# Optimization experiments

Hardware: AMD Instinct MI355X
Metric: run time of the kernel (lower is better)

Reference implementation:

```python
import jax, jax.numpy as jnp
import numpy as np

N_NODES = 100000
N_EDGES = 1600000
N_GRAPHS = 1024
EMB = 32
HID = 64
N_CLASSES = 10
N_SHAPE = 16
N_COLOR = 8


def setup_inputs() -> dict:
    key = jax.random.key(0)
    ks = jax.random.split(key, 12)
    shape_id = jax.random.randint(ks[0], (N_NODES,), 0, N_SHAPE + 1, dtype=jnp.int32)
    color_id = jax.random.randint(ks[1], (N_NODES,), 0, N_COLOR + 1, dtype=jnp.int32)
    edge_index = jax.random.randint(ks[2], (2, N_EDGES), 0, N_NODES, dtype=jnp.int32)
    batch = jnp.sort(jax.random.randint(ks[3], (N_NODES,), 0, N_GRAPHS, dtype=jnp.int32))
    shape_table = jax.random.normal(ks[4], (N_SHAPE + 1, EMB), jnp.float32)
    color_table = jax.random.normal(ks[5], (N_COLOR + 1, EMB), jnp.float32)
    W1 = jax.random.normal(ks[6], (EMB, HID), jnp.float32) / np.sqrt(EMB)
    b1 = jnp.zeros((HID,), jnp.float32)
    W2 = jax.random.normal(ks[7], (HID, HID), jnp.float32) / np.sqrt(HID)
    b2 = jnp.zeros((HID,), jnp.float32)
    Wl = jax.random.normal(ks[8], (HID, N_CLASSES), jnp.float32) / np.sqrt(HID)
    bl = jnp.zeros((N_CLASSES,), jnp.float32)
    return dict(shape_id=shape_id, color_id=color_id, edge_index=edge_index, batch=batch,
                shape_table=shape_table, color_table=color_table,
                W1=W1, b1=b1, W2=W2, b2=b2, Wl=Wl, bl=bl)


def gcn_conv(x, W, b, src, dst, num_nodes):
    # PyG GCNConv: add self-loops, symmetric normalization D^-1/2 (A+I) D^-1/2
    h = x @ W  # [N, out]
    deg = 1.0 + jax.ops.segment_sum(jnp.ones_like(dst, jnp.float32), dst, num_segments=num_nodes)
    dis = jax.lax.rsqrt(deg)  # deg >= 1 due to self-loop
    norm = dis[src] * dis[dst]  # [E]
    agg = jax.ops.segment_sum(h[src] * norm[:, None], dst, num_segments=num_nodes)
    agg = agg + h * (dis * dis)[:, None]  # self-loop term
    return agg + b


def reference(shape_id, color_id, edge_index, batch, shape_table, color_table,
              W1, b1, W2, b2, Wl, bl):
    # padding_idx=0 -> row 0 contributes zeros
    st = shape_table.at[0].set(0.0)
    ct = color_table.at[0].set(0.0)
    x = st[shape_id] + ct[color_id]  # [N, emb]
    src, dst = edge_index[0], edge_index[1]
    x = jax.nn.relu(gcn_conv(x, W1, b1, src, dst, N_NODES))
    x = jax.nn.relu(gcn_conv(x, W2, b2, src, dst, N_NODES))
    # global_mean_pool over batch ids
    sums = jax.ops.segment_sum(x, batch, num_segments=N_GRAPHS)
    cnts = jax.ops.segment_sum(jnp.ones((x.shape[0],), x.dtype), batch, num_segments=N_GRAPHS)
    pooled = sums / jnp.maximum(cnts, 1.0)[:, None]  # [B, hidden]
    return pooled @ Wl + bl  # [B, num_classes]
```

## Files before the change

### kernel.cpp

```cpp
#include <hip/hip_runtime.h>
#include <hip/hip_bf16.h>
#include <hip/hip_fp16.h>

#define N_NODES   100000
#define N_EDGES   1600000
#define N_GRAPHS  1024
#define EMB       32
#define HID       64
#define N_CLASSES 10
#define SCAN_BLOCKS 391
#define NCOMBO 153
#define BUCK_NODES 448
#define NBUCK 224
#define BIN_CAP 8192
#define EPB 4096
#define PBCAP 11328
#define SENTINEL N_NODES
#define NTILES 6250
#define AGG_GRID 3125

typedef _Float16 f16x8 __attribute__((ext_vector_type(8)));
typedef float f32x4 __attribute__((ext_vector_type(4)));

__global__ __launch_bounds__(256) void prep_kernel(
    const int* __restrict__ sid, const int* __restrict__ cid,
    const int* __restrict__ batch, int* __restrict__ combo, int* __restrict__ gstart,
    const float* __restrict__ st, const float* __restrict__ ct,
    const float* __restrict__ W1, __half* __restrict__ TCh,
    float* __restrict__ pooled, int* __restrict__ gcur, __half* __restrict__ h2s) {
    int t = threadIdx.x;
    int v = blockIdx.x * 256 + t;
    if (v < N_GRAPHS * HID) pooled[v] = 0.0f;
    if (blockIdx.x == 0) {
        if (t < NBUCK) gcur[t] = 0;
        if (t == 0) combo[N_NODES] = 0;
        if (t < 32) ((float*)(h2s + (size_t)N_NODES * HID))[t] = 0.0f;
    }
    if (v < N_NODES) {
        combo[v] = sid[v] * 9 + cid[v];
        int b = batch[v];
        int bp = (v == 0) ? -1 : batch[v - 1];
        for (int g = bp + 1; g <= b; ++g) gstart[g] = v;
        if (v == N_NODES - 1) {
            for (int g = b + 1; g <= N_GRAPHS; ++g) gstart[g] = N_NODES;
        }
    }
    if (blockIdx.x < NCOMBO && t >= 64 && t < 128) {
        int r = blockIdx.x, j = t - 64;
        int s = r / 9, c = r % 9;
        float acc = 0.0f;
        if (s != 0) {
#pragma unroll
            for (int k = 0; k < EMB; ++k) acc = fmaf(st[s * EMB + k], W1[k * HID + j], acc);
        }
        if (c != 0) {
#pragma unroll
            for (int k = 0; k < EMB; ++k) acc = fmaf(ct[c * EMB + k], W1[k * HID + j], acc);
        }
        TCh[r * HID + j] = __float2half_rn(acc);
    }
}

__global__ __launch_bounds__(512) void binA_kernel(
    const int* __restrict__ src, const int* __restrict__ dst,
    int* __restrict__ gcur, int* __restrict__ gbin) {
    __shared__ int2 stg[EPB];
    __shared__ int hist[NBUCK];
    __shared__ int base[NBUCK + 1];
    __shared__ int gstart[NBUCK];
    __shared__ int scanbuf[256];
    int t = threadIdx.x;
    int e0 = blockIdx.x * EPB;
    for (int i = t; i < NBUCK; i += 512) hist[i] = 0;
    __syncthreads();

    int2 myq[8];
    int mybo[8];
    if (e0 + EPB <= N_EDGES) {
        int eb = e0 + t * 8;
        int4 sa4 = *(const int4*)&src[eb];
        int4 sb4 = *(const int4*)&src[eb + 4];
        int4 da4 = *(const int4*)&dst[eb];
        int4 db4 = *(const int4*)&dst[eb + 4];
        int ss[8] = {sa4.x, sa4.y, sa4.z, sa4.w, sb4.x, sb4.y, sb4.z, sb4.w};
        int dd[8] = {da4.x, da4.y, da4.z, da4.w, db4.x, db4.y, db4.z, db4.w};
#pragma unroll
        for (int i = 0; i < 8; ++i) {
            unsigned b = (unsigned)dd[i] / BUCK_NODES;
            int off = atomicAdd(&hist[b], 1);
            myq[i].x = ss[i];
            myq[i].y = dd[i];
            mybo[i] = (int)(b << 16) | off;
        }
    } else {
#pragma unroll
        for (int i = 0; i < 8; ++i) {
            int e = e0 + t * 8 + i;
            if (e < N_EDGES) {
                int d = dst[e];
                unsigned b = (unsigned)d / BUCK_NODES;
                int off = atomicAdd(&hist[b], 1);
                myq[i].x = src[e];
                myq[i].y = d;
                mybo[i] = (int)(b << 16) | off;
            } else {
                mybo[i] = -1;
            }
        }
    }
    __syncthreads();

    int h = (t < NBUCK) ? hist[t] : 0;
    if (t < 256) scanbuf[t] = h;
    __syncthreads();
#pragma unroll
    for (int off = 1; off < 256; off <<= 1) {
        int x = (t < 256 && t >= off) ? scanbuf[t - off] : 0;
        __syncthreads();
        if (t < 256) scanbuf[t] += x;
        __syncthreads();
    }
    if (t < NBUCK) base[t] = scanbuf[t] - h;
    if (t == 0) base[NBUCK] = scanbuf[255];
    __syncthreads();
#pragma unroll
    for (int i = 0; i < 8; ++i) {
        if (mybo[i] >= 0) {
            int b = mybo[i] >> 16, off = mybo[i] & 0xFFFF;
            stg[base[b] + off] = myq[i];
        }
    }
    if (t < NBUCK) {
        int n = hist[t];
        gstart[t] = n ? atomicAdd(&gcur[t], n) : 0;
    }
    __syncthreads();
    int total = base[NBUCK];
    for (int i = t; i < total; i += 512) {
        int2 q = stg[i];
        unsigned b = (unsigned)q.y / BUCK_NODES;
        int local = q.y - (int)b * BUCK_NODES;
        gbin[(size_t)b * BIN_CAP + gstart[b] + (i - base[b])] = q.x | (local << 17);
    }
}

__global__ __launch_bounds__(1024) void bucket_scatter_kernel(
    const int* __restrict__ gbin, const int* __restrict__ gcur,
    float* __restrict__ dis, int* __restrict__ rowptr, int* __restrict__ epack4) {
    __shared__ __align__(16) int pbin[BIN_CAP];
    __shared__ int ldeg[BUCK_NODES];
    __shared__ int rbase[BUCK_NODES];
    __shared__ int s[512];
    int b = blockIdx.x, t = threadIdx.x;
    for (int i = t; i < BUCK_NODES; i += 1024) ldeg[i] = 0;
    __syncthreads();
    int n = gcur[b];
    int nc = (n + 3) >> 2;
    {
        const int4* my4 = (const int4*)(gbin + (size_t)b * BIN_CAP);
        for (int c = t; c < nc; c += 1024) {
            int4 p4 = my4[c];
            ((int4*)pbin)[c] = p4;
            int i0 = c * 4;
            if (i0 + 0 < n) atomicAdd(&ldeg[(unsigned)p4.x >> 17], 1);
            if (i0 + 1 < n) atomicAdd(&ldeg[(unsigned)p4.y >> 17], 1);
            if (i0 + 2 < n) atomicAdd(&ldeg[(unsigned)p4.z >> 17], 1);
            if (i0 + 3 < n) atomicAdd(&ldeg[(unsigned)p4.w >> 17], 1);
        }
    }
    __syncthreads();
    int d = (t < BUCK_NODES) ? ldeg[t] : 0;
    int v = b * BUCK_NODES + t;
    if (t < BUCK_NODES && v < N_NODES) dis[v] = rsqrtf(1.0f + (float)d);
    if (b == 0 && t == 0) dis[N_NODES] = 0.0f;
    int dp = (d + 7) & ~7;
    if (dp > 248) dp = 248;
    if (t < 512) s[t] = dp;
    __syncthreads();
#pragma unroll
    for (int off = 1; off < 512; off <<= 1) {
        int x = (t < 512 && t >= off) ? s[t - off] : 0;
        __syncthreads();
        if (t < 512) s[t] += x;
        __syncthreads();
    }
    int rp = 0;
    if (t < 512) rp = b * PBCAP + s[t] - dp;
    if (t < BUCK_NODES) {
        rbase[t] = rp;
        if (v < N_NODES) rowptr[v] = rp | (dp << 24);
    }
    for (int i = t; i < BUCK_NODES; i += 1024) ldeg[i] = 0;
    __syncthreads();
    if (t < BUCK_NODES) {
        for (int k = d; k < dp; ++k) epack4[rp + k] = SENTINEL;
    }
    for (int i = t; i < n; i += 1024) {
        int p = pbin[i];
        int local = (unsigned)p >> 17;
        int r = atomicAdd(&ldeg[local], 1);
        if (r < 248) epack4[rbase[local] + r] = p & 0x1FFFF;
    }
}

#define AGG_CHUNK(CQ, DQ, LBASE)                                               \
    _Pragma("unroll")                                                          \
    for (int i = 0; i < 8; ++i) {                                              \
        int off = __builtin_amdgcn_readlane((CQ), (LBASE) + i);                \
        int wb  = __builtin_amdgcn_readlane(__float_as_int(DQ), (LBASE) + i);  \
        __half tv = *(const __half*)((const char*)TCs + (off + lane2));        \
        acc = fmaf(__int_as_float(wb), __half2float(tv), acc);                 \
    }

#define AGG_NODE(N, RP, DEG, DV, CO)                                           \
    {                                                                          \
        int deg = (DEG);                                                       \
        int cnt = deg > 32 ? 32 : deg;                                         \
        float acc = 0.0f;                                                      \
        if (cnt > 0)  { AGG_CHUNK(cq1, dq1, (N)*16) }                          \
        if (cnt > 8)  { AGG_CHUNK(cq1, dq1, (N)*16 + 8) }                      \
        if (cnt > 16) { AGG_CHUNK(cq2, dq2, (N)*16) }                          \
        if (cnt > 24) { AGG_CHUNK(cq2, dq2, (N)*16 + 8) }                      \
        if (deg > 32) {                                                        \
            for (int e = (RP) + 32; e < (RP) + deg; ++e) {                     \
                int qx = epack4[e] & 0x1FFFF;                                  \
                float dw = dis[qx];                                            \
                __half tv = *(const __half*)((const char*)TCs +                \
                                             ((combo[qx] << 7) + lane2));      \
                acc = fmaf(dw, __half2float(tv), acc);                         \
            }                                                                  \
        }                                                                      \
        __half hv = *(const __half*)((const char*)TCs + ((CO) + lane2));       \
        float val = (DV) * fmaf(__half2float(hv), (DV), acc) + bias;           \
        val = val > 0.0f ? val : 0.0f;                                         \
        xsA[w * 4 + (N)][lane] = __float2half_rn(val * (DV));                  \
    }

__global__ __launch_bounds__(256, 7) void agg1_mm2_kernel(
    const int* __restrict__ epack4, const int* __restrict__ rowptr,
    const int* __restrict__ combo, const float* __restrict__ dis,
    const __half* __restrict__ TCh, const float* __restrict__ W2,
    const float* __restrict__ b1, __half* __restrict__ h2s) {
    __shared__ __align__(16) __half TCs[NCOMBO * HID];
    __shared__ __align__(16) __half xsA[16][72];
    int t = threadIdx.x;
    int lane = t & 63, w = t >> 6;
    int lane2 = lane * 2;
    int sub = lane >> 4, sl = lane & 15;

    int tile = blockIdx.x;
    int v0 = tile * 16 + w * 4;
    {
    }
    int rb = rowptr[v0 + sub] & 0xFFFFFF;
    int q1x = epack4[rb + sl] & 0x1FFFF;
    int q2x = epack4[rb + 16 + sl] & 0x1FFFF;
    float dq1 = dis[q1x], dq2 = dis[q2x];
    int cq1 = combo[q1x] << 7, cq2 = combo[q2x] << 7;
    int r0p = __builtin_amdgcn_readfirstlane(rowptr[v0]);
    int r1p = __builtin_amdgcn_readfirstlane(rowptr[v0 + 1]);
    int r2p = __builtin_amdgcn_readfirstlane(rowptr[v0 + 2]);
    int r3p = __builtin_amdgcn_readfirstlane(rowptr[v0 + 3]);
    float d0 = dis[v0], d1 = dis[v0 + 1], d2 = dis[v0 + 2], d3 = dis[v0 + 3];
    int o0 = combo[v0] << 7, o1 = combo[v0 + 1] << 7;
    int o2 = combo[v0 + 2] << 7, o3 = combo[v0 + 3] << 7;

    float bias = b1[lane];
    f16x8 bf0, bf1;
    {
        int colw = (w << 4) + (lane & 15);
        int kb = (lane >> 4) * 8;
#pragma unroll
        for (int i = 0; i < 8; ++i) {
            bf0[i] = (_Float16)W2[(kb + i) * HID + colw];
            bf1[i] = (_Float16)W2[(32 + kb + i) * HID + colw];
        }
    }
    {
        const int4* s4 = (const int4*)TCh;
        int4* dd4 = (int4*)TCs;
        for (int i = t; i < NCOMBO * HID * 2 / 16; i += 256) dd4[i] = s4[i];
    }
    __syncthreads();

    for (;;) {
        int ntile = tile + AGG_GRID;
        bool more = ntile < NTILES;
        int nv0 = 0, nq1x = 0, nq2x = 0;
        int nr0p = 0, nr1p = 0, nr2p = 0, nr3p = 0;
        float ndq1 = 0.0f, ndq2 = 0.0f, nd0 = 0.0f, nd1 = 0.0f, nd2 = 0.0f, nd3 = 0.0f;
        int ncq1 = 0, ncq2 = 0, no0 = 0, no1 = 0, no2 = 0, no3 = 0;
        if (more) {
            nv0 = ntile * 16 + w * 4;
            int nrb = rowptr[nv0 + sub] & 0xFFFFFF;
            nq1x = epack4[nrb + sl] & 0x1FFFF;
            nq2x = epack4[nrb + 16 + sl] & 0x1FFFF;
            ndq1 = dis[nq1x]; ndq2 = dis[nq2x];
            ncq1 = combo[nq1x] << 7; ncq2 = combo[nq2x] << 7;
            nr0p = __builtin_amdgcn_readfirstlane(rowptr[nv0]);
            nr1p = __builtin_amdgcn_readfirstlane(rowptr[nv0 + 1]);
            nr2p = __builtin_amdgcn_readfirstlane(rowptr[nv0 + 2]);
            nr3p = __builtin_amdgcn_readfirstlane(rowptr[nv0 + 3]);
            nd0 = dis[nv0]; nd1 = dis[nv0 + 1]; nd2 = dis[nv0 + 2]; nd3 = dis[nv0 + 3];
            no0 = combo[nv0] << 7; no1 = combo[nv0 + 1] << 7;
            no2 = combo[nv0 + 2] << 7; no3 = combo[nv0 + 3] << 7;
        }
        int r0 = r0p & 0xFFFFFF, g0 = (int)((unsigned)r0p >> 24);
        int r1 = r1p & 0xFFFFFF, g1 = (int)((unsigned)r1p >> 24);
        int r2 = r2p & 0xFFFFFF, g2 = (int)((unsigned)r2p >> 24);
        int r3 = r3p & 0xFFFFFF, g3 = (int)((unsigned)r3p >> 24);
        AGG_NODE(0, r0, g0, d0, o0)
        AGG_NODE(1, r1, g1, d1, o1)
        AGG_NODE(2, r2, g2, d2, o2)
        AGG_NODE(3, r3, g3, d3, o3)
        __syncthreads();

        const __half* xa = &xsA[lane & 15][0];
        f16x8 a0 = *(const f16x8*)(xa + (lane >> 4) * 8);
        f16x8 a1 = *(const f16x8*)(xa + 32 + (lane >> 4) * 8);
        __syncthreads();
        f32x4 dacc = {0.0f, 0.0f, 0.0f, 0.0f};
        dacc = __builtin_amdgcn_mfma_f32_16x16x32_f16(a0, bf0, dacc, 0, 0, 0);
        dacc = __builtin_amdgcn_mfma_f32_16x16x32_f16(a1, bf1, dacc, 0, 0, 0);

        __half* Dst = (__half*)xsA;
        {
            int colg = (w << 4) + (lane & 15);
#pragma unroll
            for (int i = 0; i < 4; ++i)
                Dst[((lane >> 4) * 4 + i) * 64 + colg] = __float2half_rn(dacc[i]);
        }
        __syncthreads();

        {
            const uint2* ds2 = (const uint2*)Dst;
            uint2* go = (uint2*)(h2s + (size_t)tile * 16 * HID);
            go[t] = ds2[t];
        }
        if (!more) break;
        __syncthreads();
        tile = ntile; v0 = nv0;
        q1x = nq1x; q2x = nq2x; dq1 = ndq1; dq2 = ndq2; cq1 = ncq1; cq2 = ncq2;
        r0p = nr0p; r1p = nr1p; r2p = nr2p; r3p = nr3p;
        d0 = nd0; d1 = nd1; d2 = nd2; d3 = nd3;
        o0 = no0; o1 = no1; o2 = no2; o3 = no3;
    }
}

__device__ __forceinline__ float agg2_node(const int* __restrict__ epack4, int sx,
                                           int rs, int deg, int lane, int lane2,
                                           const __half* __restrict__ h2s) {
    float acc = 0.0f;
    int p = rs;
    int re = rs + deg;
    for (;;) {
        int avail = re - p;
        int cnt = avail > 64 ? 64 : avail;
        int vo = sx << 7;
        int j = 0;
        for (; j + 16 <= cnt; j += 16) {
            float g[16];
#pragma unroll
            for (int i = 0; i < 16; ++i) {
                int off = __builtin_amdgcn_readlane(vo, j + i);
                g[i] = __half2float(*(const __half*)((const char*)h2s + (off + lane2)));
            }
#pragma unroll
            for (int i = 0; i < 16; ++i) acc += g[i];
        }
        if (j < cnt) {
            float g[8];
#pragma unroll
            for (int i = 0; i < 8; ++i) {
                int off = __builtin_amdgcn_readlane(vo, j + i);
                g[i] = __half2float(*(const __half*)((const char*)h2s + (off + lane2)));
            }
#pragma unroll
            for (int i = 0; i < 8; ++i) acc += g[i];
        }
        p += 64;
        if (p >= re) break;
        sx = epack4[p + lane];
    }
    return acc;
}

__global__ __launch_bounds__(256, 8) void agg2_pool_kernel(
    const int* __restrict__ epack4, const int* __restrict__ rowptr,
    const __half* __restrict__ h2s, const float* __restrict__ dis,
    const float* __restrict__ b2, const int* __restrict__ batch,
    float* __restrict__ pooled) {
    int t = threadIdx.x, lane = t & 63, w = t >> 6;
    int lane2 = lane * 2;
    int v0 = (blockIdx.x * 4 + w) * 4;

    int r0p = __builtin_amdgcn_readfirstlane(rowptr[v0]);
    int r1p = __builtin_amdgcn_readfirstlane(rowptr[v0 + 1]);
    int r2p = __builtin_amdgcn_readfirstlane(rowptr[v0 + 2]);
    int r3p = __builtin_amdgcn_readfirstlane(rowptr[v0 + 3]);
    int r0 = r0p & 0xFFFFFF, dp0 = (int)((unsigned)r0p >> 24);
    int r1 = r1p & 0xFFFFFF, dp1 = (int)((unsigned)r1p >> 24);
    int r2 = r2p & 0xFFFFFF, dp2 = (int)((unsigned)r2p >> 24);
    int r3 = r3p & 0xFFFFFF, dp3 = (int)((unsigned)r3p >> 24);

    int sa = epack4[r0 + lane];
    int sb = epack4[r1 + lane];
    int sc = epack4[r2 + lane];
    int sd = epack4[r3 + lane];

    float bv = b2[lane];
    float acc0 = agg2_node(epack4, sa, r0, dp0, lane, lane2, h2s);
    float acc1 = agg2_node(epack4, sb, r1, dp1, lane, lane2, h2s);
    float acc2 = agg2_node(epack4, sc, r2, dp2, lane, lane2, h2s);
    float acc3 = agg2_node(epack4, sd, r3, dp3, lane, lane2, h2s);

#define AGG2_VAL(V, ACC, OUT)                                                  \
    {                                                                          \
        float dv = dis[V];                                                     \
        float self = __half2float(h2s[(size_t)(V) * HID + lane]);              \
        float val = dv * ((ACC) + self) + bv;                                  \
        OUT = val > 0.0f ? val : 0.0f;                                         \
    }
    float val0, val1, val2, val3;
    AGG2_VAL(v0, acc0, val0)
    AGG2_VAL(v0 + 1, acc1, val1)
    AGG2_VAL(v0 + 2, acc2, val2)
    AGG2_VAL(v0 + 3, acc3, val3)
#undef AGG2_VAL

    int g0 = __builtin_amdgcn_readfirstlane(batch[v0]);
    int g1 = __builtin_amdgcn_readfirstlane(batch[v0 + 1]);
    int g2 = __builtin_amdgcn_readfirstlane(batch[v0 + 2]);
    int g3 = __builtin_amdgcn_readfirstlane(batch[v0 + 3]);
    float s = val0; int g = g0;
    if (g1 == g) { s += val1; } else { unsafeAtomicAdd(&pooled[g * HID + lane], s); g = g1; s = val1; }
    if (g2 == g) { s += val2; } else { unsafeAtomicAdd(&pooled[g * HID + lane], s); g = g2; s = val2; }
    if (g3 == g) { s += val3; } else { unsafeAtomicAdd(&pooled[g * HID + lane], s); g = g3; s = val3; }
    unsafeAtomicAdd(&pooled[g * HID + lane], s);
}

__global__ __launch_bounds__(64) void logits_kernel(
    const float* __restrict__ pooled, const int* __restrict__ gstart,
    const float* __restrict__ Wl, const float* __restrict__ bl,
    float* __restrict__ out) {
    __shared__ float row[HID];
    int g = blockIdx.x, t = threadIdx.x;
    int c = gstart[g + 1] - gstart[g]; if (c < 1) c = 1;
    row[t] = pooled[g * HID + t] / (float)c;
    __syncthreads();
    if (t < N_CLASSES) {
        float acc = bl[t];
#pragma unroll
        for (int k = 0; k < HID; ++k) acc = fmaf(row[k], Wl[k * N_CLASSES + t], acc);
        out[g * N_CLASSES + t] = acc;
    }
}

extern "C" void kernel_launch(void* const* d_in, const int* in_sizes, int n_in,
                              void* d_out, int out_size, void* d_ws, size_t ws_size,
                              hipStream_t stream) {
    const int*   shape_id = (const int*)d_in[0];
    const int*   color_id = (const int*)d_in[1];
    const int*   edge_idx = (const int*)d_in[2];
    const int*   batch    = (const int*)d_in[3];
    const float* st       = (const float*)d_in[4];
    const float* ct       = (const float*)d_in[5];
    const float* W1       = (const float*)d_in[6];
    const float* b1       = (const float*)d_in[7];
    const float* W2       = (const float*)d_in[8];
    const float* b2       = (const float*)d_in[9];
    const float* Wl       = (const float*)d_in[10];
    const float* bl       = (const float*)d_in[11];
    float* out = (float*)d_out;

    const int* src = edge_idx;
    const int* dst = edge_idx + N_EDGES;

    char* ws = (char*)d_ws;
    int*    combo   = (int*)   (ws + 0);
    float*  dis     = (float*) (ws + 400384);
    int*    gstart  = (int*)   (ws + 801792);
    int*    rowptr  = (int*)   (ws + 1201152);
    __half* TCh     = (__half*)(ws + 1603584);
    float*  pooled  = (float*) (ws + 1623552);
    int*    gcur    = (int*)   (ws + 1889792);
    int*    epack4  = (int*)   (ws + 1890816);
    int*    gbin    = (int*)   (ws + 14690816);
    __half* h2s     = (__half*)(ws + 29370880);

    prep_kernel<<<SCAN_BLOCKS, 256, 0, stream>>>(shape_id, color_id, batch, combo, gstart,
                                                 st, ct, W1, TCh, pooled, gcur, h2s);

    binA_kernel<<<(N_EDGES + EPB - 1) / EPB, 512, 0, stream>>>(src, dst, gcur, gbin);

    bucket_scatter_kernel<<<NBUCK, 1024, 0, stream>>>(gbin, gcur, dis, rowptr, epack4);

    agg1_mm2_kernel<<<AGG_GRID, 256, 0, stream>>>(epack4, rowptr, combo, dis, TCh, W2, b1, h2s);

    agg2_pool_kernel<<<6250, 256, 0, stream>>>(epack4, rowptr, h2s, dis, b2, batch, pooled);

    logits_kernel<<<N_GRAPHS, 64, 0, stream>>>(pooled, gstart, Wl, bl, out);
}
```

Baseline: 176.1 us.

## Aggregate four nodes' edges as one contiguous stream in both GCN aggregation kernels

Both aggregation kernels now treat the padded edge rows of a warp's four nodes as one contiguous range. They process it in 64-edge windows, routing each 8-edge chunk sum to the owning node's accumulator via prefix offsets, and prefetch the next window's indices. This replaces per-node loops, the fixed 32-entry preload, and a separate overflow path. Fewer epack loads and less per-node branching are expected, at the cost of assuming the four rows are adjacent in memory and adding per-chunk selection logic.

```diff
diff --git a/kernel.cpp b/kernel.cpp
--- a/kernel.cpp
+++ b/kernel.cpp
@@ -203,39 +203,6 @@
     }
 }
 
-#define AGG_CHUNK(CQ, DQ, LBASE)                                               \
-    _Pragma("unroll")                                                          \
-    for (int i = 0; i < 8; ++i) {                                              \
-        int off = __builtin_amdgcn_readlane((CQ), (LBASE) + i);                \
-        int wb  = __builtin_amdgcn_readlane(__float_as_int(DQ), (LBASE) + i);  \
-        __half tv = *(const __half*)((const char*)TCs + (off + lane2));        \
-        acc = fmaf(__int_as_float(wb), __half2float(tv), acc);                 \
-    }
-
-#define AGG_NODE(N, RP, DEG, DV, CO)                                           \
-    {                                                                          \
-        int deg = (DEG);                                                       \
-        int cnt = deg > 32 ? 32 : deg;                                         \
-        float acc = 0.0f;                                                      \
-        if (cnt > 0)  { AGG_CHUNK(cq1, dq1, (N)*16) }                          \
-        if (cnt > 8)  { AGG_CHUNK(cq1, dq1, (N)*16 + 8) }                      \
-        if (cnt > 16) { AGG_CHUNK(cq2, dq2, (N)*16) }                          \
-        if (cnt > 24) { AGG_CHUNK(cq2, dq2, (N)*16 + 8) }                      \
-        if (deg > 32) {                                                        \
-            for (int e = (RP) + 32; e < (RP) + deg; ++e) {                     \
-                int qx = epack4[e] & 0x1FFFF;                                  \
-                float dw = dis[qx];                                            \
-                __half tv = *(const __half*)((const char*)TCs +                \
-                                             ((combo[qx] << 7) + lane2));      \
-                acc = fmaf(dw, __half2float(tv), acc);                         \
-            }                                                                  \
-        }                                                                      \
-        __half hv = *(const __half*)((const char*)TCs + ((CO) + lane2));       \
-        float val = (DV) * fmaf(__half2float(hv), (DV), acc) + bias;           \
-        val = val > 0.0f ? val : 0.0f;                                         \
-        xsA[w * 4 + (N)][lane] = __float2half_rn(val * (DV));                  \
-    }
-
 __global__ __launch_bounds__(256, 7) void agg1_mm2_kernel(
     const int* __restrict__ epack4, const int* __restrict__ rowptr,
     const int* __restrict__ combo, const float* __restrict__ dis,
@@ -246,21 +213,18 @@
     int t = threadIdx.x;
     int lane = t & 63, w = t >> 6;
     int lane2 = lane * 2;
-    int sub = lane >> 4, sl = lane & 15;
 
     int tile = blockIdx.x;
     int v0 = tile * 16 + w * 4;
-    {
-    }
-    int rb = rowptr[v0 + sub] & 0xFFFFFF;
-    int q1x = epack4[rb + sl] & 0x1FFFF;
-    int q2x = epack4[rb + 16 + sl] & 0x1FFFF;
-    float dq1 = dis[q1x], dq2 = dis[q2x];
-    int cq1 = combo[q1x] << 7, cq2 = combo[q2x] << 7;
+
     int r0p = __builtin_amdgcn_readfirstlane(rowptr[v0]);
     int r1p = __builtin_amdgcn_readfirstlane(rowptr[v0 + 1]);
     int r2p = __builtin_amdgcn_readfirstlane(rowptr[v0 + 2]);
     int r3p = __builtin_amdgcn_readfirstlane(rowptr[v0 + 3]);
+    int r0 = r0p & 0xFFFFFF;
+    int sx0 = epack4[r0 + lane] & 0x1FFFF;
+    float dq = dis[sx0];
+    int cq = combo[sx0] << 7;
     float d0 = dis[v0], d1 = dis[v0 + 1], d2 = dis[v0 + 2], d3 = dis[v0 + 3];
     int o0 = combo[v0] << 7, o1 = combo[v0 + 1] << 7;
     int o2 = combo[v0 + 2] << 7, o3 = combo[v0 + 3] << 7;
@@ -285,43 +249,89 @@
 
     for (;;) {
         int ntile = tile + AGG_GRID;
-        bool more = ntile < NTILES;
-        int nv0 = 0, nq1x = 0, nq2x = 0;
-        int nr0p = 0, nr1p = 0, nr2p = 0, nr3p = 0;
-        float ndq1 = 0.0f, ndq2 = 0.0f, nd0 = 0.0f, nd1 = 0.0f, nd2 = 0.0f, nd3 = 0.0f;
-        int ncq1 = 0, ncq2 = 0, no0 = 0, no1 = 0, no2 = 0, no3 = 0;
-        if (more) {
+        bool moreT = ntile < NTILES;
+        int nv0 = 0, nr0p = 0, nr1p = 0, nr2p = 0, nr3p = 0, ncq0 = 0;
+        float ndq0 = 0.0f, nd0 = 0.0f, nd1 = 0.0f, nd2 = 0.0f, nd3 = 0.0f;
+        int no0 = 0, no1 = 0, no2 = 0, no3 = 0;
+        if (moreT) {
             nv0 = ntile * 16 + w * 4;
-            int nrb = rowptr[nv0 + sub] & 0xFFFFFF;
-            nq1x = epack4[nrb + sl] & 0x1FFFF;
-            nq2x = epack4[nrb + 16 + sl] & 0x1FFFF;
-            ndq1 = dis[nq1x]; ndq2 = dis[nq2x];
-            ncq1 = combo[nq1x] << 7; ncq2 = combo[nq2x] << 7;
             nr0p = __builtin_amdgcn_readfirstlane(rowptr[nv0]);
             nr1p = __builtin_amdgcn_readfirstlane(rowptr[nv0 + 1]);
             nr2p = __builtin_amdgcn_readfirstlane(rowptr[nv0 + 2]);
             nr3p = __builtin_amdgcn_readfirstlane(rowptr[nv0 + 3]);
+            int nr0 = nr0p & 0xFFFFFF;
+            int nsx0 = epack4[nr0 + lane] & 0x1FFFF;
+            ndq0 = dis[nsx0];
+            ncq0 = combo[nsx0] << 7;
             nd0 = dis[nv0]; nd1 = dis[nv0 + 1]; nd2 = dis[nv0 + 2]; nd3 = dis[nv0 + 3];
             no0 = combo[nv0] << 7; no1 = combo[nv0 + 1] << 7;
             no2 = combo[nv0 + 2] << 7; no3 = combo[nv0 + 3] << 7;
         }
-        int r0 = r0p & 0xFFFFFF, g0 = (int)((unsigned)r0p >> 24);
-        int r1 = r1p & 0xFFFFFF, g1 = (int)((unsigned)r1p >> 24);
-        int r2 = r2p & 0xFFFFFF, g2 = (int)((unsigned)r2p >> 24);
-        int r3 = r3p & 0xFFFFFF, g3 = (int)((unsigned)r3p >> 24);
-        AGG_NODE(0, r0, g0, d0, o0)
-        AGG_NODE(1, r1, g1, d1, o1)
-        AGG_NODE(2, r2, g2, d2, o2)
-        AGG_NODE(3, r3, g3, d3, o3)
+        int dp0 = (int)((unsigned)r0p >> 24);
+        int dp1 = (int)((unsigned)r1p >> 24);
+        int dp2 = (int)((unsigned)r2p >> 24);
+        int dp3 = (int)((unsigned)r3p >> 24);
+        int t1 = dp0, t2 = t1 + dp1, t3 = t2 + dp2, D = t3 + dp3;
+        float a0 = 0.0f, a1 = 0.0f, a2 = 0.0f, a3 = 0.0f;
+        float cdq = dq;
+        int ccq = cq;
+        int p = 0;
+        while (p < D) {
+            int wcnt = D - p; if (wcnt > 64) wcnt = 64;
+            bool moreW = p + 64 < D;
+            float ndq = 0.0f; int ncq = 0;
+            if (moreW) {
+                int nsx = epack4[r0 + p + 64 + lane] & 0x1FFFF;
+                ndq = dis[nsx];
+                ncq = combo[nsx] << 7;
+            }
+            for (int j = 0; j < wcnt; j += 8) {
+                float s = 0.0f;
+#pragma unroll
+                for (int i = 0; i < 8; ++i) {
+                    int off = __builtin_amdgcn_readlane(ccq, j + i);
+                    int wb  = __builtin_amdgcn_readlane(__float_as_int(cdq), j + i);
+                    __half tv = *(const __half*)((const char*)TCs + (off + lane2));
+                    s = fmaf(__int_as_float(wb), __half2float(tv), s);
+                }
+                int e0 = p + j;
+                if (e0 < t1) a0 += s;
+                else if (e0 < t2) a1 += s;
+                else if (e0 < t3) a2 += s;
+                else a3 += s;
+            }
+            p += 64;
+            cdq = ndq; ccq = ncq;
+        }
+        {
+            __half hv = *(const __half*)((const char*)TCs + (o0 + lane2));
+            float val = d0 * fmaf(__half2float(hv), d0, a0) + bias;
+            xsA[w * 4 + 0][lane] = __float2half_rn((val > 0.0f ? val : 0.0f) * d0);
+        }
+        {
+            __half hv = *(const __half*)((const char*)TCs + (o1 + lane2));
+            float val = d1 * fmaf(__half2float(hv), d1, a1) + bias;
+            xsA[w * 4 + 1][lane] = __float2half_rn((val > 0.0f ? val : 0.0f) * d1);
+        }
+        {
+            __half hv = *(const __half*)((const char*)TCs + (o2 + lane2));
+            float val = d2 * fmaf(__half2float(hv), d2, a2) + bias;
+            xsA[w * 4 + 2][lane] = __float2half_rn((val > 0.0f ? val : 0.0f) * d2);
+        }
+        {
+            __half hv = *(const __half*)((const char*)TCs + (o3 + lane2));
+            float val = d3 * fmaf(__half2float(hv), d3, a3) + bias;
+            xsA[w * 4 + 3][lane] = __float2half_rn((val > 0.0f ? val : 0.0f) * d3);
+        }
         __syncthreads();
 
         const __half* xa = &xsA[lane & 15][0];
-        f16x8 a0 = *(const f16x8*)(xa + (lane >> 4) * 8);
-        f16x8 a1 = *(const f16x8*)(xa + 32 + (lane >> 4) * 8);
+        f16x8 a0f = *(const f16x8*)(xa + (lane >> 4) * 8);
+        f16x8 a1f = *(const f16x8*)(xa + 32 + (lane >> 4) * 8);
         __syncthreads();
         f32x4 dacc = {0.0f, 0.0f, 0.0f, 0.0f};
-        dacc = __builtin_amdgcn_mfma_f32_16x16x32_f16(a0, bf0, dacc, 0, 0, 0);
-        dacc = __builtin_amdgcn_mfma_f32_16x16x32_f16(a1, bf1, dacc, 0, 0, 0);
+        dacc = __builtin_amdgcn_mfma_f32_16x16x32_f16(a0f, bf0, dacc, 0, 0, 0);
+        dacc = __builtin_amdgcn_mfma_f32_16x16x32_f16(a1f, bf1, dacc, 0, 0, 0);
 
         __half* Dst = (__half*)xsA;
         {
@@ -337,52 +347,15 @@
             uint2* go = (uint2*)(h2s + (size_t)tile * 16 * HID);
             go[t] = ds2[t];
         }
-        if (!more) break;
+        if (!moreT) break;
         __syncthreads();
         tile = ntile; v0 = nv0;
-        q1x = nq1x; q2x = nq2x; dq1 = ndq1; dq2 = ndq2; cq1 = ncq1; cq2 = ncq2;
         r0p = nr0p; r1p = nr1p; r2p = nr2p; r3p = nr3p;
+        r0 = r0p & 0xFFFFFF;
+        dq = ndq0; cq = ncq0;
         d0 = nd0; d1 = nd1; d2 = nd2; d3 = nd3;
         o0 = no0; o1 = no1; o2 = no2; o3 = no3;
     }
-}
-
-__device__ __forceinline__ float agg2_node(const int* __restrict__ epack4, int sx,
-                                           int rs, int deg, int lane, int lane2,
-                                           const __half* __restrict__ h2s) {
-    float acc = 0.0f;
-    int p = rs;
-    int re = rs + deg;
-    for (;;) {
-        int avail = re - p;
-        int cnt = avail > 64 ? 64 : avail;
-        int vo = sx << 7;
-        int j = 0;
-        for (; j + 16 <= cnt; j += 16) {
-            float g[16];
-#pragma unroll
-            for (int i = 0; i < 16; ++i) {
-                int off = __builtin_amdgcn_readlane(vo, j + i);
-                g[i] = __half2float(*(const __half*)((const char*)h2s + (off + lane2)));
-            }
-#pragma unroll
-            for (int i = 0; i < 16; ++i) acc += g[i];
-        }
-        if (j < cnt) {
-            float g[8];
-#pragma unroll
-            for (int i = 0; i < 8; ++i) {
-                int off = __builtin_amdgcn_readlane(vo, j + i);
-                g[i] = __half2float(*(const __half*)((const char*)h2s + (off + lane2)));
-            }
-#pragma unroll
-            for (int i = 0; i < 8; ++i) acc += g[i];
-        }
-        p += 64;
-        if (p >= re) break;
-        sx = epack4[p + lane];
-    }
-    return acc;
 }
 
 __global__ __launch_bounds__(256, 8) void agg2_pool_kernel(
@@ -398,22 +371,64 @@
     int r1p = __builtin_amdgcn_readfirstlane(rowptr[v0 + 1]);
     int r2p = __builtin_amdgcn_readfirstlane(rowptr[v0 + 2]);
     int r3p = __builtin_amdgcn_readfirstlane(rowptr[v0 + 3]);
-    int r0 = r0p & 0xFFFFFF, dp0 = (int)((unsigned)r0p >> 24);
-    int r1 = r1p & 0xFFFFFF, dp1 = (int)((unsigned)r1p >> 24);
-    int r2 = r2p & 0xFFFFFF, dp2 = (int)((unsigned)r2p >> 24);
-    int r3 = r3p & 0xFFFFFF, dp3 = (int)((unsigned)r3p >> 24);
-
-    int sa = epack4[r0 + lane];
-    int sb = epack4[r1 + lane];
-    int sc = epack4[r2 + lane];
-    int sd = epack4[r3 + lane];
+    int r0 = r0p & 0xFFFFFF;
+    int dp0 = (int)((unsigned)r0p >> 24);
+    int dp1 = (int)((unsigned)r1p >> 24);
+    int dp2 = (int)((unsigned)r2p >> 24);
+    int dp3 = (int)((unsigned)r3p >> 24);
+    int t1 = dp0, t2 = t1 + dp1, t3 = t2 + dp2, D = t3 + dp3;
+
+    float a0 = 0.0f, a1 = 0.0f, a2 = 0.0f, a3 = 0.0f;
+    if (D > 0) {
+        int sx = epack4[r0 + lane] & 0x1FFFF;
+        int p = 0;
+        for (;;) {
+            int wcnt = D - p; if (wcnt > 64) wcnt = 64;
+            int vo = sx << 7;
+            bool more = p + 64 < D;
+            int nsx = 0;
+            if (more) nsx = epack4[r0 + p + 64 + lane] & 0x1FFFF;
+            int j = 0;
+            for (; j + 16 <= wcnt; j += 16) {
+                float g[16];
+#pragma unroll
+                for (int i = 0; i < 16; ++i) {
+                    int off = __builtin_amdgcn_readlane(vo, j + i);
+                    g[i] = __half2float(*(const __half*)((const char*)h2s + (off + lane2)));
+                }
+                float s0 = g[0];
+#pragma unroll
+                for (int i = 1; i < 8; ++i) s0 += g[i];
+                float s1 = g[8];
+#pragma unroll
+                for (int i = 9; i < 16; ++i) s1 += g[i];
+                int e0 = p + j, e1 = p + j + 8;
+                if (e0 < t1) a0 += s0; else if (e0 < t2) a1 += s0;
+                else if (e0 < t3) a2 += s0; else a3 += s0;
+                if (e1 < t1) a0 += s1; else if (e1 < t2) a1 += s1;
+                else if (e1 < t3) a2 += s1; else a3 += s1;
+            }
+            for (; j < wcnt; j += 8) {
+                float g[8];
+#pragma unroll
+                for (int i = 0; i < 8; ++i) {
+                    int off = __builtin_amdgcn_readlane(vo, j + i);
+                    g[i] = __half2float(*(const __half*)((const char*)h2s + (off + lane2)));
+                }
+                float s0 = g[0];
+#pragma unroll
+                for (int i = 1; i < 8; ++i) s0 += g[i];
+                int e0 = p + j;
+                if (e0 < t1) a0 += s0; else if (e0 < t2) a1 += s0;
+                else if (e0 < t3) a2 += s0; else a3 += s0;
+            }
+            p += 64;
+            if (!more) break;
+            sx = nsx;
+        }
+    }
 
     float bv = b2[lane];
-    float acc0 = agg2_node(epack4, sa, r0, dp0, lane, lane2, h2s);
-    float acc1 = agg2_node(epack4, sb, r1, dp1, lane, lane2, h2s);
-    float acc2 = agg2_node(epack4, sc, r2, dp2, lane, lane2, h2s);
-    float acc3 = agg2_node(epack4, sd, r3, dp3, lane, lane2, h2s);
-
 #define AGG2_VAL(V, ACC, OUT)                                                  \
     {                                                                          \
         float dv = dis[V];                                                     \
@@ -422,10 +437,10 @@
         OUT = val > 0.0f ? val : 0.0f;                                         \
     }
     float val0, val1, val2, val3;
-    AGG2_VAL(v0, acc0, val0)
-    AGG2_VAL(v0 + 1, acc1, val1)
-    AGG2_VAL(v0 + 2, acc2, val2)
-    AGG2_VAL(v0 + 3, acc3, val3)
+    AGG2_VAL(v0, a0, val0)
+    AGG2_VAL(v0 + 1, a1, val1)
+    AGG2_VAL(v0 + 2, a2, val2)
+    AGG2_VAL(v0 + 3, a3, val3)
 #undef AGG2_VAL
 
     int g0 = __builtin_amdgcn_readfirstlane(batch[v0]);
```

Measured after the change: 190.6 us. 1.08x slower.
